# Kernel optimization log

Hardware: AMD Instinct MI355X
Metric: run time of the kernel (lower is better)

Reference implementation:

```python
import jax, jax.numpy as jnp
import numpy as np


def setup_inputs() -> dict:
    key = jax.random.key(0)
    x = jax.random.normal(key, (16, 64, 256, 256), dtype=jnp.float32)
    return {"x": x}


def reference(x):
    # x: [B, C, H, W]
    b, c, h, w = x.shape
    # L2 norm over channel dim -> [B, 1, H, W]
    weights = jnp.sqrt(jnp.sum(x * x, axis=1, keepdims=True))
    # softmax over height (dim=2)
    weights = jax.nn.softmax(weights, axis=2)
    # weighted sum over height -> [B, C, 1, W]
    weighted_sum = jnp.sum(x * weights, axis=2, keepdims=True)
    weight_sum = jnp.sum(weights, axis=2, keepdims=True)  # [B, 1, 1, W]
    compressed = weighted_sum / (weight_sum + 1e-8)
    # broadcast-repeat along height -> [B, C, H, W]
    out = jnp.broadcast_to(compressed, (b, c, h, w))
    return out
```

## Files before the change

kernel.cpp:

```cpp
#include <hip/hip_runtime.h>


constexpr int B = 16, C = 64, H = 256, W = 256, W4 = 64;
constexpr int HC = 32;
constexpr int HPC = H / HC;
constexpr float KSUB = 8.0f;

typedef float nfloat4 __attribute__((ext_vector_type(4)));

__device__ __forceinline__ float4 f4add(float4 a, float4 b) {
    return make_float4(a.x + b.x, a.y + b.y, a.z + b.z, a.w + b.w);
}

__global__ __launch_bounds__(256) void k_pass1(const float* __restrict__ x,
                                               float4* __restrict__ pcomp,
                                               float4* __restrict__ pden) {
    __shared__ float4 red[2][4][64];
    int blk = blockIdx.x;
    int b = blk >> 5, hc = blk & 31;
    int t = threadIdx.x, cq = t >> 6, w4 = t & 63;
    int h0 = hc * HPC;

    const float4* xb = (const float4*)x + ((size_t)(b * C + cq * 16) * H + h0) * W4 + w4;

    float4 acc[16];
#pragma unroll
    for (int j = 0; j < 16; ++j) acc[j] = make_float4(0.f, 0.f, 0.f, 0.f);
    float4 dacc = make_float4(0.f, 0.f, 0.f, 0.f);

    for (int hh = 0; hh < HPC; ++hh) {
        float4 xv[16];
        float4 ps = make_float4(0.f, 0.f, 0.f, 0.f);
#pragma unroll
        for (int j = 0; j < 16; ++j) {
            xv[j] = xb[(size_t)j * H * W4 + (size_t)hh * W4];
            ps.x += xv[j].x * xv[j].x; ps.y += xv[j].y * xv[j].y;
            ps.z += xv[j].z * xv[j].z; ps.w += xv[j].w * xv[j].w;
        }
        red[hh & 1][cq][w4] = ps;
        __syncthreads();
        float4 s = f4add(f4add(red[hh & 1][0][w4], red[hh & 1][1][w4]),
                         f4add(red[hh & 1][2][w4], red[hh & 1][3][w4]));
        float4 e = make_float4(__expf(sqrtf(s.x) - KSUB), __expf(sqrtf(s.y) - KSUB),
                               __expf(sqrtf(s.z) - KSUB), __expf(sqrtf(s.w) - KSUB));
        if (cq == 0) dacc = f4add(dacc, e);
#pragma unroll
        for (int j = 0; j < 16; ++j) {
            acc[j].x += xv[j].x * e.x; acc[j].y += xv[j].y * e.y;
            acc[j].z += xv[j].z * e.z; acc[j].w += xv[j].w * e.w;
        }
    }

    size_t pc = ((size_t)(b * HC + hc) * C + cq * 16) * W4 + w4;
#pragma unroll
    for (int j = 0; j < 16; ++j)
        pcomp[pc + (size_t)j * W4] = acc[j];
    if (cq == 0)
        pden[(size_t)(b * HC + hc) * W4 + w4] = dacc;
}

__global__ __launch_bounds__(256) void k_pass2(const float4* __restrict__ pcomp,
                                               const float4* __restrict__ pden,
                                               float* __restrict__ out) {
    __shared__ float4 redc[4][64], redd[4][64];
    __shared__ float4 fin[64];
    int blk = blockIdx.x;
    int b = blk >> 6, c = blk & 63;
    int t = threadIdx.x, hq = t >> 6, w4 = t & 63;

    float4 sc = make_float4(0.f, 0.f, 0.f, 0.f), sd = sc;
#pragma unroll
    for (int k = 0; k < 8; ++k) {
        int hc = hq * 8 + k;
        sc = f4add(sc, pcomp[((size_t)(b * HC + hc) * C + c) * W4 + w4]);
        sd = f4add(sd, pden[(size_t)(b * HC + hc) * W4 + w4]);
    }
    redc[hq][w4] = sc;
    redd[hq][w4] = sd;
    __syncthreads();
    if (hq == 0) {
        float4 Cs = f4add(f4add(redc[0][w4], redc[1][w4]), f4add(redc[2][w4], redc[3][w4]));
        float4 Ds = f4add(f4add(redd[0][w4], redd[1][w4]), f4add(redd[2][w4], redd[3][w4]));
        fin[w4] = make_float4(Cs.x / (Ds.x * (1.0f + 1e-8f)),
                              Cs.y / (Ds.y * (1.0f + 1e-8f)),
                              Cs.z / (Ds.z * (1.0f + 1e-8f)),
                              Cs.w / (Ds.w * (1.0f + 1e-8f)));
    }
    __syncthreads();
    float4 fv = fin[t & 63];
    nfloat4 f = { fv.x, fv.y, fv.z, fv.w };
    nfloat4* op = (nfloat4*)out + (size_t)(b * C + c) * H * W4;
    for (int i = t; i < H * W4; i += 256)
        __builtin_nontemporal_store(f, op + i);
}

extern "C" void kernel_launch(void* const* d_in, const int* in_sizes, int n_in,
                              void* d_out, int out_size, void* d_ws, size_t ws_size,
                              hipStream_t stream) {
    const float* x = (const float*)d_in[0];
    float* out = (float*)d_out;
    float4* pcomp = (float4*)d_ws;
    float4* pden  = pcomp + (size_t)B * HC * C * W4;

    k_pass1<<<B * HC, 256, 0, stream>>>(x, pcomp, pden);
    k_pass2<<<B * C,  256, 0, stream>>>(pcomp, pden, out);
}
```

Baseline: 460.0 us.

## Double the pass-1 block to 512 threads, prefetch the next row, use plain stores

Pass 1 now uses 512 threads per block, so each thread handles 8 channels instead of 16. Loads for the next height row go into a second register buffer while the current row is reduced, which is meant to hide global memory latency behind the barrier. The output writes in pass 2 change from nontemporal stores to ordinary float4 stores. The tradeoffs are a longer cross-warp reduction over 8 slices, a larger block, and different cache behavior for a 268MB output write.

```diff
diff --git a/kernel.cpp b/kernel.cpp
--- a/kernel.cpp
+++ b/kernel.cpp
@@ -6,54 +6,64 @@
 constexpr int HPC = H / HC;
 constexpr float KSUB = 8.0f;
 
-typedef float nfloat4 __attribute__((ext_vector_type(4)));
-
 __device__ __forceinline__ float4 f4add(float4 a, float4 b) {
     return make_float4(a.x + b.x, a.y + b.y, a.z + b.z, a.w + b.w);
 }
 
-__global__ __launch_bounds__(256) void k_pass1(const float* __restrict__ x,
+__global__ __launch_bounds__(512) void k_pass1(const float* __restrict__ x,
                                                float4* __restrict__ pcomp,
                                                float4* __restrict__ pden) {
-    __shared__ float4 red[2][4][64];
+    __shared__ float4 red[2][8][64];
     int blk = blockIdx.x;
     int b = blk >> 5, hc = blk & 31;
     int t = threadIdx.x, cq = t >> 6, w4 = t & 63;
     int h0 = hc * HPC;
 
-    const float4* xb = (const float4*)x + ((size_t)(b * C + cq * 16) * H + h0) * W4 + w4;
+    const float4* xb = (const float4*)x + ((size_t)(b * C + cq * 8) * H + h0) * W4 + w4;
+    const size_t cstride = (size_t)H * W4;
 
-    float4 acc[16];
+    float4 acc[8];
 #pragma unroll
-    for (int j = 0; j < 16; ++j) acc[j] = make_float4(0.f, 0.f, 0.f, 0.f);
+    for (int j = 0; j < 8; ++j) acc[j] = make_float4(0.f, 0.f, 0.f, 0.f);
     float4 dacc = make_float4(0.f, 0.f, 0.f, 0.f);
 
+    float4 xva[8], xvb[8];
+#pragma unroll
+    for (int j = 0; j < 8; ++j) xva[j] = xb[j * cstride];
+
+#pragma unroll
     for (int hh = 0; hh < HPC; ++hh) {
-        float4 xv[16];
+        float4* cur = (hh & 1) ? xvb : xva;
+        float4* nxt = (hh & 1) ? xva : xvb;
+        if (hh + 1 < HPC) {
+#pragma unroll
+            for (int j = 0; j < 8; ++j)
+                nxt[j] = xb[j * cstride + (size_t)(hh + 1) * W4];
+        }
         float4 ps = make_float4(0.f, 0.f, 0.f, 0.f);
 #pragma unroll
-        for (int j = 0; j < 16; ++j) {
-            xv[j] = xb[(size_t)j * H * W4 + (size_t)hh * W4];
-            ps.x += xv[j].x * xv[j].x; ps.y += xv[j].y * xv[j].y;
-            ps.z += xv[j].z * xv[j].z; ps.w += xv[j].w * xv[j].w;
+        for (int j = 0; j < 8; ++j) {
+            ps.x += cur[j].x * cur[j].x; ps.y += cur[j].y * cur[j].y;
+            ps.z += cur[j].z * cur[j].z; ps.w += cur[j].w * cur[j].w;
         }
         red[hh & 1][cq][w4] = ps;
         __syncthreads();
-        float4 s = f4add(f4add(red[hh & 1][0][w4], red[hh & 1][1][w4]),
-                         f4add(red[hh & 1][2][w4], red[hh & 1][3][w4]));
+        float4 s = red[hh & 1][0][w4];
+#pragma unroll
+        for (int k = 1; k < 8; ++k) s = f4add(s, red[hh & 1][k][w4]);
         float4 e = make_float4(__expf(sqrtf(s.x) - KSUB), __expf(sqrtf(s.y) - KSUB),
                                __expf(sqrtf(s.z) - KSUB), __expf(sqrtf(s.w) - KSUB));
         if (cq == 0) dacc = f4add(dacc, e);
 #pragma unroll
-        for (int j = 0; j < 16; ++j) {
-            acc[j].x += xv[j].x * e.x; acc[j].y += xv[j].y * e.y;
-            acc[j].z += xv[j].z * e.z; acc[j].w += xv[j].w * e.w;
+        for (int j = 0; j < 8; ++j) {
+            acc[j].x += cur[j].x * e.x; acc[j].y += cur[j].y * e.y;
+            acc[j].z += cur[j].z * e.z; acc[j].w += cur[j].w * e.w;
         }
     }
 
-    size_t pc = ((size_t)(b * HC + hc) * C + cq * 16) * W4 + w4;
+    size_t pc = ((size_t)(b * HC + hc) * C + cq * 8) * W4 + w4;
 #pragma unroll
-    for (int j = 0; j < 16; ++j)
+    for (int j = 0; j < 8; ++j)
         pcomp[pc + (size_t)j * W4] = acc[j];
     if (cq == 0)
         pden[(size_t)(b * HC + hc) * W4 + w4] = dacc;
@@ -88,10 +98,9 @@
     }
     __syncthreads();
     float4 fv = fin[t & 63];
-    nfloat4 f = { fv.x, fv.y, fv.z, fv.w };
-    nfloat4* op = (nfloat4*)out + (size_t)(b * C + c) * H * W4;
+    float4* op = (float4*)out + (size_t)(b * C + c) * H * W4;
     for (int i = t; i < H * W4; i += 256)
-        __builtin_nontemporal_store(f, op + i);
+        op[i] = fv;
 }
 
 extern "C" void kernel_launch(void* const* d_in, const int* in_sizes, int n_in,
@@ -102,6 +111,6 @@
     float4* pcomp = (float4*)d_ws;
     float4* pden  = pcomp + (size_t)B * HC * C * W4;
 
-    k_pass1<<<B * HC, 256, 0, stream>>>(x, pcomp, pden);
+    k_pass1<<<B * HC, 512, 0, stream>>>(x, pcomp, pden);
     k_pass2<<<B * C,  256, 0, stream>>>(pcomp, pden, out);
 }
```

New measurement: 468.9 us. About the same (+1.9%).
